# Optimization experiments

Hardware: AMD Instinct MI355X
Metric: run time of the kernel (lower is better)

## Reference

```python
import jax, jax.numpy as jnp
import numpy as np

KERNEL = 7  # median blur window size (odd)


def setup_inputs() -> dict:
    key = jax.random.key(0)
    # NCHW image batch, values in [0,1) like normalized images
    img = jax.random.uniform(key, (8, 3, 512, 512), dtype=jnp.float32)
    return {"img": img}


def _median_blur(img, k):
    # Matches kornia.filters.median_blur: zero padding ('same'), then median
    # over the k*k window. k*k is odd so the exact middle of the sorted
    # window equals torch.median's lower median.
    pad = k // 2
    b, c, h, w = img.shape
    x = jnp.pad(img, ((0, 0), (0, 0), (pad, pad), (pad, pad)))  # zero pad
    # unfold: [B, C, k*k, H, W] — same materialization as kornia's conv2d
    # with binary one-hot kernels. Loop is over the fixed k*k = 49 taps.
    patches = jnp.stack(
        [x[:, :, i:i + h, j:j + w] for i in range(k) for j in range(k)],
        axis=2,
    )
    mid = (k * k) // 2
    return jnp.sort(patches, axis=2)[:, :, mid]  # [B, C, H, W]


def reference(img):
    return _median_blur(img, KERNEL)
```

## Files before the change

### kernel.cpp

```cpp
#include <hip/hip_runtime.h>
#include <utility>

#define IMG_H 512
#define IMG_W 512

typedef _Float16 h2 __attribute__((ext_vector_type(2)));

__device__ __forceinline__ h2 h2min(h2 a, h2 b) { return __builtin_elementwise_min(a, b); }
__device__ __forceinline__ h2 h2max(h2 a, h2 b) { return __builtin_elementwise_max(a, b); }

struct Op { int kind, a, b, c; };
constexpr int NSLOT = 512;
constexpr int MAXOPS = 4096;
struct Prog { Op ops[MAXOPS]; int n; int nphys; bool ok; };

constexpr int pow2ceil(int x) { int p = 1; while (p < x) p += p; return p; }

struct Run { int s[48]; int len; };

struct Builder {
    Op ops[MAXOPS] = {};
    int n = 0;
    int nv = 0;
    bool ok = true;

    constexpr void emit(int k, int a, int b, int c) {
        if (n < MAXOPS) ops[n++] = Op{k, a, b, c}; else ok = false;
    }
    constexpr int fresh() {
        if (nv < NSLOT) return nv++;
        ok = false; return 0;
    }
    constexpr Run load_col(int c) {
        Run r{}; r.len = 7;
        for (int i = 0; i < 7; ++i) { r.s[i] = fresh(); emit(2, r.s[i], c * 7 + i, 0); }
        for (int p = 1; p < 7; p += p)
            for (int k = p; k > 0; k /= 2)
                for (int j = k % p; j + k < 7; j += k + k)
                    for (int i = 0; i < k; ++i)
                        if (i + j + k < 7 && (i + j) / (p + p) == (i + j + k) / (p + p))
                            emit(0, r.s[i + j], r.s[i + j + k], 0);
        return r;
    }
    constexpr Run copy(const Run& a) {
        Run r{}; r.len = a.len;
        for (int i = 0; i < a.len; ++i) { r.s[i] = fresh(); emit(1, r.s[i], a.s[i], 0); }
        return r;
    }
    constexpr Run merge(const Run& A, const Run& B) {
        int P = pow2ceil(A.len > B.len ? A.len : B.len);
        if (A.len > P || B.len > P || 2 * P > 96) { ok = false; }
        int map[96] = {};
        for (int i = 0; i < 2 * P; ++i) map[i] = -1;
        for (int i = 0; i < A.len; ++i) map[i] = A.s[i];
        for (int i = 0; i < B.len; ++i) map[P + i] = B.s[i];
        for (int k = P; k > 0; k /= 2)
            for (int j = k % P; j + k < 2 * P; j += k + k)
                for (int i = 0; i < k; ++i) {
                    int x = i + j, y = i + j + k;
                    int a = map[x], b = map[y];
                    if (a >= 0 && b >= 0) emit(0, a, b, 0);
                    else if (a < 0 && b >= 0) { map[x] = b; map[y] = -1; }
                }
        Run r{}; r.len = A.len + B.len;
        for (int i = 0; i < r.len; ++i) { if (map[i] < 0) ok = false; r.s[i] = map[i]; }
        for (int i = r.len; i < 2 * P; ++i) if (map[i] >= 0) ok = false;
        return r;
    }
    constexpr void select49(const Run& A, const Run& B, int o) {
        if (A.len != 42 || B.len != 7) ok = false;
        int T[7] = {};
        for (int t = 0; t < 7; ++t) {
            T[t] = fresh();
            emit(7, A.s[17 + t], B.s[6 - t], T[t]);
        }
        emit(4, T[0], T[1], 0); emit(4, T[2], T[3], 0);
        emit(4, T[4], T[5], 0); emit(4, T[6], A.s[24], 0);
        emit(4, T[0], T[2], 0); emit(4, T[4], T[6], 0);
        emit(4, T[0], T[4], 0);
        emit(3, o, T[0], 0);
    }
};

constexpr Prog build() {
    Builder b{};
    Run g1 = b.load_col(1), g2 = b.load_col(2), g3 = b.load_col(3),
        g4 = b.load_col(4), g5 = b.load_col(5), g6 = b.load_col(6),
        g7 = b.load_col(7), g8 = b.load_col(8);
    Run g2c = b.copy(g2), g4c = b.copy(g4), g6c = b.copy(g6);

    Run M12 = b.merge(g1, g2c);
    Run M34 = b.merge(g3, g4c);
    Run M56 = b.merge(g5, g6c);
    Run M56b = b.copy(M56);
    Run C28A = b.merge(M34, M56);
    Run C28Ac = b.copy(C28A);
    Run C42A = b.merge(C28Ac, M12);
    Run g0 = b.load_col(0);
    b.select49(C42A, g0, 0);
    b.select49(C42A, g7, 1);

    Run M78 = b.merge(g7, g8);
    Run M78b = b.copy(M78);
    Run C42B = b.merge(C28A, M78);
    Run g9 = b.load_col(9);
    b.select49(C42B, g2, 2);
    b.select49(C42B, g9, 3);

    Run g10 = b.load_col(10);
    Run M910 = b.merge(g9, g10);
    Run C28B = b.merge(M78b, M910);
    Run C28Bc = b.copy(C28B);
    Run C42C = b.merge(C28Bc, M56b);
    Run g11 = b.load_col(11);
    b.select49(C42C, g4, 4);
    b.select49(C42C, g11, 5);

    Run g12 = b.load_col(12);
    Run M1112 = b.merge(g11, g12);
    Run C42D = b.merge(C28B, M1112);
    Run g13 = b.load_col(13);
    b.select49(C42D, g6, 6);
    b.select49(C42D, g13, 7);

    Prog p{};
    bool needed[NSLOT] = {};
    int kindr[MAXOPS] = {};
    bool keep[MAXOPS] = {};
    for (int t = b.n - 1; t >= 0; --t) {
        Op o = b.ops[t];
        if (o.kind == 3) { keep[t] = true; kindr[t] = 3; needed[o.b] = true; }
        else if (o.kind == 0) {
            bool na = needed[o.a], nb = needed[o.b];
            if (na && nb)      { keep[t] = true; kindr[t] = 0; }
            else if (na)       { keep[t] = true; kindr[t] = 4; needed[o.b] = true; }
            else if (nb)       { keep[t] = true; kindr[t] = 5; needed[o.a] = true; }
        } else if (o.kind == 1) {
            if (needed[o.a]) { keep[t] = true; kindr[t] = 1; needed[o.a] = false; needed[o.b] = true; }
        } else if (o.kind == 2) {
            if (needed[o.a]) { keep[t] = true; kindr[t] = 2; needed[o.a] = false; }
        } else if (o.kind == 4) {
            if (needed[o.a]) { keep[t] = true; kindr[t] = 4; needed[o.b] = true; }
        } else if (o.kind == 5) {
            if (needed[o.b]) { keep[t] = true; kindr[t] = 5; needed[o.a] = true; }
        } else if (o.kind == 7) {
            if (needed[o.c]) { keep[t] = true; kindr[t] = 7; needed[o.c] = false;
                               needed[o.a] = true; needed[o.b] = true; }
        }
    }
    p.n = 0;
    for (int t = 0; t < b.n; ++t)
        if (keep[t]) { p.ops[p.n] = b.ops[t]; p.ops[p.n].kind = kindr[t]; ++p.n; }
    p.ok = b.ok;

    bool live[NSLOT] = {};
    bool lu_a[MAXOPS] = {};
    bool lu_b[MAXOPS] = {};
    for (int t = p.n - 1; t >= 0; --t) {
        Op o = p.ops[t];
        if (o.kind == 0 || o.kind == 4 || o.kind == 5 || o.kind == 7) {
            lu_a[t] = !live[o.a]; lu_b[t] = !live[o.b];
        } else if (o.kind == 1 || o.kind == 3) {
            lu_b[t] = !live[o.b];
        }
        if (o.kind == 0) { live[o.a] = false; live[o.b] = false; }
        else if (o.kind == 1 || o.kind == 2 || o.kind == 4) live[o.a] = false;
        else if (o.kind == 5) live[o.b] = false;
        else if (o.kind == 7) live[o.c] = false;
        if (o.kind == 0 || o.kind == 4 || o.kind == 5 || o.kind == 7) {
            live[o.a] = true; live[o.b] = true;
        } else if (o.kind == 1 || o.kind == 3) live[o.b] = true;
    }
    for (int t = 0; t < p.n; ++t) {
        Op o = p.ops[t];
        if (o.kind == 0 && (lu_a[t] || lu_b[t])) p.ok = false;
        if (o.kind == 4 && lu_a[t]) p.ok = false;
        if (o.kind == 5 && lu_b[t]) p.ok = false;
    }
    int phys[NSLOT] = {};
    bool bound[NSLOT] = {};
    int freelist[NSLOT] = {};
    int nfree = 0, nphys = 0;
    for (int t = 0; t < p.n; ++t) {
        Op o = p.ops[t];
        if (o.kind == 0) {
            if (!bound[o.a] || !bound[o.b]) p.ok = false;
            p.ops[t].a = phys[o.a]; p.ops[t].b = phys[o.b];
        } else if (o.kind == 4) {
            if (!bound[o.a] || !bound[o.b]) p.ok = false;
            p.ops[t].a = phys[o.a]; p.ops[t].b = phys[o.b];
            if (lu_b[t]) { freelist[nfree++] = phys[o.b]; bound[o.b] = false; }
        } else if (o.kind == 5) {
            if (!bound[o.a] || !bound[o.b]) p.ok = false;
            p.ops[t].a = phys[o.a]; p.ops[t].b = phys[o.b];
            if (lu_a[t]) { freelist[nfree++] = phys[o.a]; bound[o.a] = false; }
        } else if (o.kind == 7) {
            if (!bound[o.a] || !bound[o.b]) p.ok = false;
            p.ops[t].a = phys[o.a]; p.ops[t].b = phys[o.b];
            if (lu_a[t]) { freelist[nfree++] = phys[o.a]; bound[o.a] = false; }
            if (lu_b[t]) { freelist[nfree++] = phys[o.b]; bound[o.b] = false; }
            int pc = (nfree > 0) ? freelist[--nfree] : nphys++;
            phys[o.c] = pc; bound[o.c] = true;
            p.ops[t].c = pc;
        } else if (o.kind == 1) {
            if (!bound[o.b]) p.ok = false;
            int pb = phys[o.b];
            p.ops[t].b = pb;
            if (lu_b[t]) { freelist[nfree++] = pb; bound[o.b] = false; }
            int pa = (nfree > 0) ? freelist[--nfree] : nphys++;
            phys[o.a] = pa; bound[o.a] = true;
            p.ops[t].a = pa;
        } else if (o.kind == 2) {
            int pa = (nfree > 0) ? freelist[--nfree] : nphys++;
            phys[o.a] = pa; bound[o.a] = true;
            p.ops[t].a = pa;
        } else {
            if (!bound[o.b]) p.ok = false;
            p.ops[t].b = phys[o.b];
            if (lu_b[t]) { freelist[nfree++] = phys[o.b]; bound[o.b] = false; }
        }
        if (nphys > NSLOT || nfree > NSLOT) p.ok = false;
    }
    p.nphys = nphys;
    return p;
}

constexpr Prog PROG = build();
static_assert(PROG.ok, "program build failed");
static_assert(PROG.n > 300 && PROG.n < 2400, "op count out of range");
static_assert(PROG.nphys > 0 && PROG.nphys <= 256, "regalloc blew up");

template <int P>
__device__ __forceinline__ h2& vslot(h2* v0, h2* v1, h2* v2, h2* v3) {
    if constexpr (P < 64) return v0[P];
    else if constexpr (P < 128) return v1[P - 64];
    else if constexpr (P < 192) return v2[P - 128];
    else return v3[P - 192];
}
template <int P>
__device__ __forceinline__ h2 cslot(const h2* c0, const h2* c1) {
    if constexpr (P < 49) return c0[P];
    else return c1[P - 49];
}

template <int I>
__device__ __forceinline__ void step(h2* v0, h2* v1, h2* v2, h2* v3,
                                     const h2* c0, const h2* c1, h2* med) {
    constexpr Op o = PROG.ops[I];
    if constexpr (o.kind == 0) {
        h2& A = vslot<o.a>(v0, v1, v2, v3);
        h2& B = vslot<o.b>(v0, v1, v2, v3);
        h2 lo = h2min(A, B);
        h2 hi = h2max(A, B);
        A = lo; B = hi;
    } else if constexpr (o.kind == 1) {
        vslot<o.a>(v0, v1, v2, v3) = vslot<o.b>(v0, v1, v2, v3);
    } else if constexpr (o.kind == 2) {
        vslot<o.a>(v0, v1, v2, v3) = cslot<o.b>(c0, c1);
    } else if constexpr (o.kind == 3) {
        med[o.a] = vslot<o.b>(v0, v1, v2, v3);
    } else if constexpr (o.kind == 4) {
        h2& A = vslot<o.a>(v0, v1, v2, v3);
        A = h2min(A, vslot<o.b>(v0, v1, v2, v3));
    } else if constexpr (o.kind == 5) {
        h2& B = vslot<o.b>(v0, v1, v2, v3);
        B = h2max(vslot<o.a>(v0, v1, v2, v3), B);
    } else {
        vslot<o.c>(v0, v1, v2, v3) =
            h2max(vslot<o.a>(v0, v1, v2, v3), vslot<o.b>(v0, v1, v2, v3));
    }
}

template <size_t... Is>
__device__ __forceinline__ void run_all(h2* v0, h2* v1, h2* v2, h2* v3,
                                        const h2* c0, const h2* c1, h2* med,
                                        std::index_sequence<Is...>) {
    (step<(int)Is>(v0, v1, v2, v3, c0, c1, med), ...);
}

__global__ __launch_bounds__(256, 2) void median7x7_kernel(
        const float* __restrict__ img, float* __restrict__ out) {
    const int bc = blockIdx.z;
    const int tx = threadIdx.x;
    const int ty = threadIdx.y;
    const int x0 = (blockIdx.x * 64 + tx) * 8;
    const int y  = (blockIdx.y * 4 + ty) * 2;

    const float* base = img + (size_t)bc * (IMG_H * IMG_W);
    const bool okl = (x0 >= 4);
    const bool okr = (x0 <= 496);
    const int xl = okl ? (x0 - 4) : 0;
    const int xr = okr ? (x0 + 8) : 504;

    h2 c0[49], c1[49];
    float prv[14];
#pragma unroll
    for (int r = 0; r < 8; ++r) {
        const int yy = y - 3 + r;
        float4 Q0, Q1, Q2, Q3;
        if ((unsigned)yy < IMG_H) {
            const float* rp = base + (size_t)yy * IMG_W;
            Q0 = *(const float4*)(rp + xl);
            Q1 = *(const float4*)(rp + x0);
            Q2 = *(const float4*)(rp + x0 + 4);
            Q3 = *(const float4*)(rp + xr);
        } else {
            Q0 = make_float4(0.f, 0.f, 0.f, 0.f); Q1 = Q0; Q2 = Q0; Q3 = Q0;
        }
        float cur[14];
        cur[0] = okl ? Q0.y : 0.f; cur[1] = okl ? Q0.z : 0.f; cur[2] = okl ? Q0.w : 0.f;
        cur[3] = Q1.x; cur[4] = Q1.y; cur[5] = Q1.z; cur[6] = Q1.w;
        cur[7] = Q2.x; cur[8] = Q2.y; cur[9] = Q2.z; cur[10] = Q2.w;
        cur[11] = okr ? Q3.x : 0.f; cur[12] = okr ? Q3.y : 0.f; cur[13] = okr ? Q3.z : 0.f;
        if (r > 0) {
#pragma unroll
            for (int c = 0; c < 14; ++c) {
                const int idx = c * 7 + (r - 1);
                h2 val = (h2)__builtin_amdgcn_cvt_pkrtz(prv[c], cur[c]);
                if (idx < 49) c0[idx] = val; else c1[idx - 49] = val;
            }
        }
#pragma unroll
        for (int c = 0; c < 14; ++c) prv[c] = cur[c];
    }

    h2 va[64], vb[64], vc[64], vd[64];
    h2 med[8];
    run_all(va, vb, vc, vd, c0, c1, med, std::make_index_sequence<(size_t)PROG.n>{});

    float* op = out + (size_t)bc * (IMG_H * IMG_W) + (size_t)y * IMG_W + x0;
    *(float4*)op = make_float4((float)med[0].x, (float)med[1].x,
                               (float)med[2].x, (float)med[3].x);
    *(float4*)(op + 4) = make_float4((float)med[4].x, (float)med[5].x,
                                     (float)med[6].x, (float)med[7].x);
    *(float4*)(op + IMG_W) = make_float4((float)med[0].y, (float)med[1].y,
                                         (float)med[2].y, (float)med[3].y);
    *(float4*)(op + IMG_W + 4) = make_float4((float)med[4].y, (float)med[5].y,
                                             (float)med[6].y, (float)med[7].y);
}

extern "C" void kernel_launch(void* const* d_in, const int* in_sizes, int n_in,
                              void* d_out, int out_size, void* d_ws, size_t ws_size,
                              hipStream_t stream) {
    const float* img = (const float*)d_in[0];
    float* out = (float*)d_out;
    dim3 grid(1, 64, 24);
    dim3 block(64, 4, 1);
    hipLaunchKernelGGL(median7x7_kernel, grid, block, 0, stream, img, out);
}
```

Before: 89.08 us.

## Stage input rows in shared-memory fp16 tile instead of per-thread global loads

Each block now cooperatively loads 14 input rows (with zero-padded halo columns) into a shared fp16 tile, converting to half once. Each thread then reads its 8 rows as 16-wide half vectors from LDS and builds the packed window pairs from them. This removes redundant overlapping global float4 loads and repeated conversions across neighbouring threads, at the cost of LDS usage, a block barrier and possible bank conflicts on the 32-byte reads.

```diff
diff --git a/kernel.cpp b/kernel.cpp
--- a/kernel.cpp
+++ b/kernel.cpp
@@ -5,6 +5,7 @@
 #define IMG_W 512
 
 typedef _Float16 h2 __attribute__((ext_vector_type(2)));
+typedef _Float16 h16 __attribute__((ext_vector_type(16)));
 
 __device__ __forceinline__ h2 h2min(h2 a, h2 b) { return __builtin_elementwise_min(a, b); }
 __device__ __forceinline__ h2 h2max(h2 a, h2 b) { return __builtin_elementwise_max(a, b); }
@@ -278,56 +279,63 @@
     (step<(int)Is>(v0, v1, v2, v3, c0, c1, med), ...);
 }
 
+#define TW 528
+
 __global__ __launch_bounds__(256, 2) void median7x7_kernel(
         const float* __restrict__ img, float* __restrict__ out) {
     const int bc = blockIdx.z;
     const int tx = threadIdx.x;
     const int ty = threadIdx.y;
-    const int x0 = (blockIdx.x * 64 + tx) * 8;
-    const int y  = (blockIdx.y * 4 + ty) * 2;
+    const int tid = ty * 64 + tx;
+    const int yb = blockIdx.y * 8;
+    const int x0 = tx * 8;
 
     const float* base = img + (size_t)bc * (IMG_H * IMG_W);
-    const bool okl = (x0 >= 4);
-    const bool okr = (x0 <= 496);
-    const int xl = okl ? (x0 - 4) : 0;
-    const int xr = okr ? (x0 + 8) : 504;
+
+    __shared__ __align__(16) _Float16 tile[14][TW];
+
+    const int col2 = tid * 2;
+#pragma unroll
+    for (int r = 0; r < 14; ++r) {
+        const int gr = yb - 3 + r;
+        float f0 = 0.f, f1 = 0.f;
+        if ((unsigned)gr < IMG_H) {
+            float2 q = *(const float2*)(base + (size_t)gr * IMG_W + col2);
+            f0 = q.x; f1 = q.y;
+        }
+        *(h2*)&tile[r][4 + col2] = (h2)__builtin_amdgcn_cvt_pkrtz(f0, f1);
+        if (tid < 8) {
+            const int hi = (tid < 2) ? 2 * tid : 512 + 2 * tid;
+            h2 z; z.x = (_Float16)0.f; z.y = (_Float16)0.f;
+            *(h2*)&tile[r][hi] = z;
+        }
+    }
+    __syncthreads();
+
+    const int lbase = ty * 2;
+    h16 row[8];
+#pragma unroll
+    for (int k = 0; k < 8; ++k)
+        row[k] = *(const h16*)&tile[lbase + k][8 * tx];
 
     h2 c0[49], c1[49];
-    float prv[14];
 #pragma unroll
-    for (int r = 0; r < 8; ++r) {
-        const int yy = y - 3 + r;
-        float4 Q0, Q1, Q2, Q3;
-        if ((unsigned)yy < IMG_H) {
-            const float* rp = base + (size_t)yy * IMG_W;
-            Q0 = *(const float4*)(rp + xl);
-            Q1 = *(const float4*)(rp + x0);
-            Q2 = *(const float4*)(rp + x0 + 4);
-            Q3 = *(const float4*)(rp + xr);
-        } else {
-            Q0 = make_float4(0.f, 0.f, 0.f, 0.f); Q1 = Q0; Q2 = Q0; Q3 = Q0;
-        }
-        float cur[14];
-        cur[0] = okl ? Q0.y : 0.f; cur[1] = okl ? Q0.z : 0.f; cur[2] = okl ? Q0.w : 0.f;
-        cur[3] = Q1.x; cur[4] = Q1.y; cur[5] = Q1.z; cur[6] = Q1.w;
-        cur[7] = Q2.x; cur[8] = Q2.y; cur[9] = Q2.z; cur[10] = Q2.w;
-        cur[11] = okr ? Q3.x : 0.f; cur[12] = okr ? Q3.y : 0.f; cur[13] = okr ? Q3.z : 0.f;
-        if (r > 0) {
+    for (int c = 0; c < 14; ++c) {
 #pragma unroll
-            for (int c = 0; c < 14; ++c) {
-                const int idx = c * 7 + (r - 1);
-                h2 val = (h2)__builtin_amdgcn_cvt_pkrtz(prv[c], cur[c]);
-                if (idx < 49) c0[idx] = val; else c1[idx - 49] = val;
-            }
-        }
-#pragma unroll
-        for (int c = 0; c < 14; ++c) prv[c] = cur[c];
+        for (int d = 0; d < 7; ++d) {
+            h2 val;
+            val.x = row[d][c + 1];
+            val.y = row[d + 1][c + 1];
+            const int idx = c * 7 + d;
+            if (idx < 49) c0[idx] = val; else c1[idx - 49] = val;
+        }
     }
 
     h2 va[64], vb[64], vc[64], vd[64];
     h2 med[8];
     run_all(va, vb, vc, vd, c0, c1, med, std::make_index_sequence<(size_t)PROG.n>{});
 
+    const int y = yb + ty * 2;
     float* op = out + (size_t)bc * (IMG_H * IMG_W) + (size_t)y * IMG_W + x0;
     *(float4*)op = make_float4((float)med[0].x, (float)med[1].x,
                                (float)med[2].x, (float)med[3].x);
```

New measurement: 96.28 us. +8.1%, slower.
